# Kernel tuning notes

Measured on AMD Instinct MI355X. Metric: run time of the kernel, lower is better.

The kernel has to match this reference:

```python
import jax, jax.numpy as jnp
import numpy as np

EPS = 1e-6
NUM_HEADS = 8
NUM_TOKENS = 196

def setup_inputs() -> dict:
    key = jax.random.key(0)
    ks = jax.random.split(key, 4)
    B, N, C = 32, 3136, 384
    H, Dh, M = NUM_HEADS, C // NUM_HEADS, NUM_TOKENS
    return {
        "x": jax.random.normal(ks[0], (B, N, C), dtype=jnp.float32),
        "q_param": jax.random.normal(ks[1], (1, M, H, Dh), dtype=jnp.float32) * 0.02,
        "kv_w": jax.random.normal(ks[2], (2 * C, C), dtype=jnp.float32) * 0.02,
        "proj_w": jax.random.normal(ks[3], (C, C), dtype=jnp.float32) * 0.02,
        "proj_b": jnp.zeros((C,), dtype=jnp.float32),
        "ln_w": jnp.ones((C,), dtype=jnp.float32),
        "ln_b": jnp.zeros((C,), dtype=jnp.float32),
    }

def reference(x, q_param, kv_w, proj_w, proj_b, ln_w, ln_b):
    B, N, C = x.shape
    H = NUM_HEADS
    Dh = C // H
    # LayerNorm (eps=1e-6)
    mu = jnp.mean(x, axis=-1, keepdims=True)
    var = jnp.mean(jnp.square(x - mu), axis=-1, keepdims=True)
    x = (x - mu) * jax.lax.rsqrt(var + EPS) * ln_w + ln_b
    # exact GELU (nn.GELU default)
    x = jax.nn.gelu(x, approximate=False)
    # kv projection (no bias): [B,N,2C] -> k,v each [B,H,N,Dh]
    kv = (x @ kv_w.T).reshape(B, N, 2, H, Dh)
    kv = jnp.transpose(kv, (2, 0, 3, 1, 4))
    k, v = kv[0], kv[1]
    # learnable queries: (1,M,H,Dh) -> (1,H,M,Dh)
    q = jnp.transpose(q_param, (0, 2, 1, 3))
    # NOTE: source applies NO 1/sqrt(Dh) scaling
    attn = jnp.einsum("bhmd,bhnd->bhmn", jnp.broadcast_to(q, (B, H, NUM_TOKENS, Dh)), k)
    attn = jax.nn.softmax(attn, axis=-1)
    out = jnp.einsum("bhmn,bhnd->bhmd", attn, v)  # [B,H,M,Dh]
    out = jnp.transpose(out, (0, 2, 1, 3)).reshape(B, NUM_TOKENS, C)
    return out @ proj_w.T + proj_b
```

## Files before the change

### kernel.cpp

```cpp
#include <hip/hip_runtime.h>
#include <stdint.h>

typedef float f32x4 __attribute__((ext_vector_type(4)));
typedef short s16x8 __attribute__((ext_vector_type(8)));
typedef short s16x4 __attribute__((ext_vector_type(4)));
typedef unsigned short ushort_t;

#define B_  32
#define N_  3136
#define C_  384
#define H_  8
#define DH_ 48
#define M_  196
#define ROWS  (B_*N_)
#define PROWS (B_*M_)

static __device__ __forceinline__ ushort_t f2bf(float f) {
  union { float f; uint32_t u; } v; v.f = f;
  uint32_t r = (v.u + 0x7fffu + ((v.u >> 16) & 1u)) >> 16;
  return (ushort_t)r;
}
static __device__ __forceinline__ ushort_t f2bf_fast(float f) {
  union { float f; uint32_t u; } v; v.f = f;
  return (ushort_t)((v.u + 0x8000u) >> 16);
}
static __device__ __forceinline__ uint32_t pkbf(float lo, float hi) {
  uint32_t r;
  asm("v_cvt_pk_bf16_f32 %0, %1, %2" : "=v"(r) : "v"(lo), "v"(hi));
  return r;
}

static __device__ __forceinline__ f32x4 mfma_16x16x32(s16x8 a, s16x8 b, f32x4 c) {
  return __builtin_amdgcn_mfma_f32_16x16x32_bf16(a, b, c, 0, 0, 0);
}

static __device__ __forceinline__ f32x4 mfma_16x16x16(s16x4 a, s16x4 b, f32x4 c) {
#if __has_builtin(__builtin_amdgcn_mfma_f32_16x16x16_bf16)
  return __builtin_amdgcn_mfma_f32_16x16x16_bf16(a, b, c, 0, 0, 0);
#elif __has_builtin(__builtin_amdgcn_mfma_f32_16x16x16bf16_1k)
  return __builtin_amdgcn_mfma_f32_16x16x16bf16_1k(a, b, c, 0, 0, 0);
#else
  f32x4 d;
  asm("v_mfma_f32_16x16x16_bf16 %0, %1, %2, %3" : "=v"(d) : "v"(a), "v"(b), "v"(c));
  return d;
#endif
}

static __device__ __forceinline__ void gload_lds16(const void* g, void* l) {
  __builtin_amdgcn_global_load_lds(
      (const __attribute__((address_space(1))) void*)(uintptr_t)g,
      (__attribute__((address_space(3))) void*)(uint32_t)(uintptr_t)l,
      16, 0, 0);
}

__global__ __launch_bounds__(256) void k_ln_gelu(
    const float* __restrict__ x, const float* __restrict__ lnw,
    const float* __restrict__ lnb, ushort_t* __restrict__ x16) {
  int row = blockIdx.x * 4 + (threadIdx.x >> 6);
  int lane = threadIdx.x & 63;
  const float2* xr = (const float2*)(x + (size_t)row * C_);
  float2 v0 = xr[lane], v1 = xr[lane + 64], v2 = xr[lane + 128];
  float s  = v0.x + v0.y + v1.x + v1.y + v2.x + v2.y;
  float ss = v0.x*v0.x + v0.y*v0.y + v1.x*v1.x + v1.y*v1.y + v2.x*v2.x + v2.y*v2.y;
#pragma unroll
  for (int off = 1; off < 64; off <<= 1) {
    s  += __shfl_xor(s, off);
    ss += __shfl_xor(ss, off);
  }
  float mu = s * (1.0f / C_);
  float rs = rsqrtf(ss * (1.0f / C_) - mu * mu + 1e-6f);
  const float2* wr = (const float2*)lnw;
  const float2* br = (const float2*)lnb;
  uint32_t* outp = (uint32_t*)(x16 + (size_t)row * C_);
#pragma unroll
  for (int t = 0; t < 3; ++t) {
    int idx = lane + t * 64;
    float2 v = (t == 0) ? v0 : ((t == 1) ? v1 : v2);
    float2 w = wr[idx], bb = br[idx];
    float a0 = (v.x - mu) * rs * w.x + bb.x;
    float a1 = (v.y - mu) * rs * w.y + bb.y;
    a0 = 0.5f * a0 * (1.0f + erff(a0 * 0.70710678118654752440f));
    a1 = 0.5f * a1 * (1.0f + erff(a1 * 0.70710678118654752440f));
    outp[idx] = (uint32_t)f2bf_fast(a0) | ((uint32_t)f2bf_fast(a1) << 16);
  }
}

__global__ __launch_bounds__(256) void k_convert(
    const float* __restrict__ kvw, const float* __restrict__ pw,
    const float* __restrict__ qp, ushort_t* __restrict__ wkv16,
    ushort_t* __restrict__ wp16, ushort_t* __restrict__ q16) {
  int i = blockIdx.x * 256 + threadIdx.x;
  if (i < 2 * C_ * C_) wkv16[i] = f2bf(kvw[i]);
  if (i < C_ * C_)     wp16[i]  = f2bf(pw[i]);
  if (i < M_ * H_ * DH_) {
    int d = i % DH_; int t = i / DH_; int h = t % H_; int m = t / H_;
    q16[((size_t)h * M_ + m) * DH_ + d] = f2bf(qp[i]);
  }
}

template <typename OutT, bool BIAS, bool SWZ>
__global__ __launch_bounds__(256) void k_gemm_bt(
    const ushort_t* __restrict__ A, const ushort_t* __restrict__ Bw,
    OutT* __restrict__ Co, const float* __restrict__ bias,
    int M, int N, int K, int ntn) {
  __shared__ ushort_t lA[3][128 * 32];
  __shared__ ushort_t lB[3][128 * 32];
  int bid = blockIdx.x;
  if (SWZ) bid = (bid & 7) * (gridDim.x >> 3) + (bid >> 3);
  int tr = bid / ntn, tc = bid % ntn;
  int tid = threadIdx.x;
  int w = tid >> 6, l = tid & 63;
  int wr = w >> 1, wc = w & 1;
  int c = l & 15, g = l >> 4;
  f32x4 acc[4][4];
#pragma unroll
  for (int i = 0; i < 4; ++i)
#pragma unroll
    for (int j = 0; j < 4; ++j) acc[i][j] = (f32x4){0.f, 0.f, 0.f, 0.f};
  const size_t a0 = (size_t)tr * 128, b0 = (size_t)tc * 128;
  int srow = l >> 2;
  int scol = (((l & 3) ^ ((l >> 3) & 3))) * 8;
  const int rsw = (c >> 1) & 3;
  const int T = K >> 5;
#pragma unroll
  for (int r = 0; r < 2; ++r) {
    int lr = w * 16 + r * 64;
    gload_lds16(A  + (a0 + lr + srow) * (size_t)K + scol, &lA[0][lr * 32]);
    gload_lds16(Bw + (b0 + lr + srow) * (size_t)K + scol, &lB[0][lr * 32]);
  }
  if (T > 1) {
#pragma unroll
    for (int r = 0; r < 2; ++r) {
      int lr = w * 16 + r * 64;
      gload_lds16(A  + (a0 + lr + srow) * (size_t)K + 32 + scol, &lA[1][lr * 32]);
      gload_lds16(Bw + (b0 + lr + srow) * (size_t)K + 32 + scol, &lB[1][lr * 32]);
    }
  }
  int cur = 0, nxt2 = 2;
  for (int t = 0; t < T; ++t) {
    if (t + 2 < T) {
      int kt = (t + 2) << 5;
#pragma unroll
      for (int r = 0; r < 2; ++r) {
        int lr = w * 16 + r * 64;
        gload_lds16(A  + (a0 + lr + srow) * (size_t)K + kt + scol, &lA[nxt2][lr * 32]);
        gload_lds16(Bw + (b0 + lr + srow) * (size_t)K + kt + scol, &lB[nxt2][lr * 32]);
      }
      asm volatile("s_waitcnt vmcnt(8)" ::: "memory");
    } else if (t + 1 < T) {
      asm volatile("s_waitcnt vmcnt(4)" ::: "memory");
    } else {
      asm volatile("s_waitcnt vmcnt(0)" ::: "memory");
    }
    __builtin_amdgcn_sched_barrier(0);
    __builtin_amdgcn_s_barrier();
    s16x8 af[4], bf[4];
#pragma unroll
    for (int i = 0; i < 4; ++i) {
      int row = wr * 64 + i * 16 + c;
      af[i] = *(const s16x8*)&lA[cur][row * 32 + ((unsigned)(g ^ rsw)) * 8];
    }
#pragma unroll
    for (int j = 0; j < 4; ++j) {
      int row = wc * 64 + j * 16 + c;
      bf[j] = *(const s16x8*)&lB[cur][row * 32 + ((unsigned)(g ^ rsw)) * 8];
    }
#pragma unroll
    for (int i = 0; i < 4; ++i)
#pragma unroll
      for (int j = 0; j < 4; ++j)
        acc[i][j] = mfma_16x16x32(af[i], bf[j], acc[i][j]);
    __builtin_amdgcn_sched_barrier(0);
    __builtin_amdgcn_s_barrier();
    cur = (cur == 2) ? 0 : cur + 1;
    nxt2 = (nxt2 == 2) ? 0 : nxt2 + 1;
  }
#pragma unroll
  for (int i = 0; i < 4; ++i) {
#pragma unroll
    for (int j = 0; j < 4; ++j) {
      size_t col = b0 + wc * 64 + j * 16 + c;
      float bs = BIAS ? bias[col] : 0.0f;
#pragma unroll
      for (int q = 0; q < 4; ++q) {
        size_t row = a0 + wr * 64 + i * 16 + g * 4 + q;
        float v = acc[i][j][q] + bs;
        if constexpr (sizeof(OutT) == 2) Co[row * N + col] = f2bf(v);
        else                             Co[row * N + col] = v;
      }
    }
  }
}

__global__ __launch_bounds__(512) void k_attn(
    const ushort_t* __restrict__ kv, const ushort_t* __restrict__ q16,
    ushort_t* __restrict__ att16) {
  int bh = blockIdx.x;
  int b = bh >> 3, h = bh & 7;
  __shared__ ushort_t Kl[2][64 * 72];
  __shared__ ushort_t Vt[2][48 * 76];
  int tid = threadIdx.x;
  int w = tid >> 6, l = tid & 63;
  int c = l & 15, g = l >> 4;
  for (int i = tid; i < 2 * 64 * 72; i += 512) ((ushort_t*)Kl)[i] = 0;
  s16x8 qf[2][2];
#pragma unroll
  for (int i = 0; i < 2; ++i)
#pragma unroll
    for (int kk = 0; kk < 2; ++kk) {
      int m = w * 32 + i * 16 + c;
      int dh = kk * 32 + g * 8;
      s16x8 z = {0, 0, 0, 0, 0, 0, 0, 0};
      qf[i][kk] = (m < M_ && dh < DH_)
                      ? *(const s16x8*)(q16 + ((size_t)h * M_ + m) * DH_ + dh)
                      : z;
    }
  f32x4 o[3][2];
#pragma unroll
  for (int f = 0; f < 3; ++f)
#pragma unroll
    for (int i = 0; i < 2; ++i) o[f][i] = (f32x4){0.f, 0.f, 0.f, 0.f};
  float rm[2] = {-3e38f, -3e38f}, rl[2] = {0.f, 0.f};
  int srow = tid >> 3, spart = tid & 7;
  const size_t rowstride = (size_t)(2 * C_);
  const size_t gbase = (size_t)b * N_ * rowstride + h * DH_ + spart * 6;
  uint32_t kr0, kr1, kr2, vr0, vr1, vr2;
  {
    const ushort_t* p = kv + gbase + (size_t)srow * rowstride;
    kr0 = *(const uint32_t*)(p);
    kr1 = *(const uint32_t*)(p + 2);
    kr2 = *(const uint32_t*)(p + 4);
    vr0 = *(const uint32_t*)(p + C_);
    vr1 = *(const uint32_t*)(p + C_ + 2);
    vr2 = *(const uint32_t*)(p + C_ + 4);
  }
  __syncthreads();

  for (int t = 0; t < 49; ++t) {
    int p = t & 1;
    uint32_t* kd = (uint32_t*)&Kl[p][srow * 72 + spart * 6];
    kd[0] = kr0; kd[1] = kr1; kd[2] = kr2;
    int dbase = spart * 6;
    ushort_t* vt = &Vt[p][0];
    vt[(dbase + 0) * 76 + srow] = (ushort_t)vr0;
    vt[(dbase + 1) * 76 + srow] = (ushort_t)(vr0 >> 16);
    vt[(dbase + 2) * 76 + srow] = (ushort_t)vr1;
    vt[(dbase + 3) * 76 + srow] = (ushort_t)(vr1 >> 16);
    vt[(dbase + 4) * 76 + srow] = (ushort_t)vr2;
    vt[(dbase + 5) * 76 + srow] = (ushort_t)(vr2 >> 16);
    __syncthreads();
    {
      int tn = (t < 48) ? t + 1 : t;
      const ushort_t* pp = kv + gbase + ((size_t)tn * 64 + srow) * rowstride;
      kr0 = *(const uint32_t*)(pp);
      kr1 = *(const uint32_t*)(pp + 2);
      kr2 = *(const uint32_t*)(pp + 4);
      vr0 = *(const uint32_t*)(pp + C_);
      vr1 = *(const uint32_t*)(pp + C_ + 2);
      vr2 = *(const uint32_t*)(pp + C_ + 4);
    }
    f32x4 s[4][2];
    __builtin_amdgcn_s_setprio(1);
#pragma unroll
    for (int j = 0; j < 4; ++j) {
      s16x8 kf0 = *(const s16x8*)&Kl[p][(j * 16 + c) * 72 + g * 8];
      s16x8 kf1 = *(const s16x8*)&Kl[p][(j * 16 + c) * 72 + 32 + g * 8];
#pragma unroll
      for (int i = 0; i < 2; ++i) {
        f32x4 z = {0.f, 0.f, 0.f, 0.f};
        f32x4 t0 = mfma_16x16x32(kf0, qf[i][0], z);
        s[j][i] = mfma_16x16x32(kf1, qf[i][1], t0);
      }
    }
    __builtin_amdgcn_s_setprio(0);
    s16x4 pb[2][4];
#pragma unroll
    for (int i = 0; i < 2; ++i) {
      float tm = s[0][i][0];
#pragma unroll
      for (int j = 0; j < 4; ++j)
#pragma unroll
        for (int q = 0; q < 4; ++q) tm = fmaxf(tm, s[j][i][q]);
      tm = fmaxf(tm, __shfl_xor(tm, 16));
      tm = fmaxf(tm, __shfl_xor(tm, 32));
      if (__any(tm > rm[i] + 8.f)) {
        float nm = fmaxf(rm[i], tm);
        float corr = __expf(rm[i] - nm);
        rl[i] *= corr;
#pragma unroll
        for (int f = 0; f < 3; ++f) o[f][i] *= corr;
        rm[i] = nm;
      }
      float m_i = rm[i];
      float ts = 0.f;
#pragma unroll
      for (int j = 0; j < 4; ++j) {
        float p0 = __expf(s[j][i][0] - m_i);
        float p1 = __expf(s[j][i][1] - m_i);
        float p2 = __expf(s[j][i][2] - m_i);
        float p3 = __expf(s[j][i][3] - m_i);
        ts += (p0 + p1) + (p2 + p3);
        uint32_t* pp = (uint32_t*)&pb[i][j];
        pp[0] = pkbf(p0, p1);
        pp[1] = pkbf(p2, p3);
      }
      ts += __shfl_xor(ts, 16);
      ts += __shfl_xor(ts, 32);
      rl[i] += ts;
    }
    __builtin_amdgcn_s_setprio(1);
#pragma unroll
    for (int f = 0; f < 3; ++f)
#pragma unroll
      for (int j = 0; j < 4; ++j) {
        s16x4 vf = *(const s16x4*)&Vt[p][(f * 16 + c) * 76 + j * 16 + g * 4];
        o[f][0] = mfma_16x16x16(vf, pb[0][j], o[f][0]);
        o[f][1] = mfma_16x16x16(vf, pb[1][j], o[f][1]);
      }
    __builtin_amdgcn_s_setprio(0);
  }
#pragma unroll
  for (int i = 0; i < 2; ++i) {
    int m = w * 32 + i * 16 + c;
    if (m < M_) {
      float inv = 1.0f / rl[i];
#pragma unroll
      for (int f = 0; f < 3; ++f) {
        uint32_t w0 = (uint32_t)f2bf_fast(o[f][i][0] * inv) |
                      ((uint32_t)f2bf_fast(o[f][i][1] * inv) << 16);
        uint32_t w1 = (uint32_t)f2bf_fast(o[f][i][2] * inv) |
                      ((uint32_t)f2bf_fast(o[f][i][3] * inv) << 16);
        uint2 val; val.x = w0; val.y = w1;
        *(uint2*)&att16[((size_t)b * M_ + m) * C_ + h * DH_ + f * 16 + g * 4] = val;
      }
    }
  }
}

extern "C" void kernel_launch(void* const* d_in, const int* in_sizes, int n_in,
                              void* d_out, int out_size, void* d_ws, size_t ws_size,
                              hipStream_t stream) {
  (void)in_sizes; (void)n_in; (void)out_size; (void)ws_size;
  const float* x   = (const float*)d_in[0];
  const float* qp  = (const float*)d_in[1];
  const float* kvw = (const float*)d_in[2];
  const float* pw  = (const float*)d_in[3];
  const float* pbv = (const float*)d_in[4];
  const float* lnw = (const float*)d_in[5];
  const float* lnb = (const float*)d_in[6];
  float* out = (float*)d_out;

  ushort_t* x16   = (ushort_t*)d_ws;
  ushort_t* kv16  = x16 + (size_t)ROWS * C_;
  ushort_t* att16 = kv16 + (size_t)ROWS * 2 * C_;
  ushort_t* wkv16 = att16 + (size_t)PROWS * C_;
  ushort_t* wp16  = wkv16 + 2 * C_ * C_;
  ushort_t* q16   = wp16 + C_ * C_;

  hipLaunchKernelGGL(k_ln_gelu, dim3(ROWS / 4), dim3(256), 0, stream, x, lnw, lnb, x16);
  hipLaunchKernelGGL(k_convert, dim3((2 * C_ * C_ + 255) / 256), dim3(256), 0, stream,
                     kvw, pw, qp, wkv16, wp16, q16);
  hipLaunchKernelGGL((k_gemm_bt<ushort_t, false, true>),
                     dim3((ROWS / 128) * (2 * C_ / 128)), dim3(256), 0, stream,
                     x16, wkv16, kv16, (const float*)nullptr, ROWS, 2 * C_, C_, 2 * C_ / 128);
  hipLaunchKernelGGL(k_attn, dim3(B_ * H_), dim3(512), 0, stream, kv16, q16, att16);
  hipLaunchKernelGGL((k_gemm_bt<float, true, false>),
                     dim3((PROWS / 128) * (C_ / 128)), dim3(256), 0, stream,
                     att16, wp16, out, pbv, PROWS, C_, C_, C_ / 128);
}
```

Baseline: 248.7 us.

## Use 64-wide K tiles with double buffering in GEMM; skip idle attention wave

The GEMM kernel moves from a three-stage pipeline of 32-wide K tiles to a two-stage pipeline of 64-wide K tiles, with a new XOR swizzle over 8 column chunks. Each barrier pair now covers two MFMA k-steps, which halves the synchronisation per unit of work at the cost of a shallower prefetch. In the attention kernel, wave 7 (query rows 224 and up, past M=196) skips the QK, softmax and PV compute but still takes part in loads and barriers, removing wasted MFMA and exp work.

```diff
diff --git a/kernel.cpp b/kernel.cpp
--- a/kernel.cpp
+++ b/kernel.cpp
@@ -103,8 +103,8 @@
     const ushort_t* __restrict__ A, const ushort_t* __restrict__ Bw,
     OutT* __restrict__ Co, const float* __restrict__ bias,
     int M, int N, int K, int ntn) {
-  __shared__ ushort_t lA[3][128 * 32];
-  __shared__ ushort_t lB[3][128 * 32];
+  __shared__ ushort_t lA[2][128 * 64];
+  __shared__ ushort_t lB[2][128 * 64];
   int bid = blockIdx.x;
   if (SWZ) bid = (bid & 7) * (gridDim.x >> 3) + (bid >> 3);
   int tr = bid / ntn, tc = bid % ntn;
@@ -118,63 +118,55 @@
 #pragma unroll
     for (int j = 0; j < 4; ++j) acc[i][j] = (f32x4){0.f, 0.f, 0.f, 0.f};
   const size_t a0 = (size_t)tr * 128, b0 = (size_t)tc * 128;
-  int srow = l >> 2;
-  int scol = (((l & 3) ^ ((l >> 3) & 3))) * 8;
-  const int rsw = (c >> 1) & 3;
-  const int T = K >> 5;
-#pragma unroll
-  for (int r = 0; r < 2; ++r) {
-    int lr = w * 16 + r * 64;
-    gload_lds16(A  + (a0 + lr + srow) * (size_t)K + scol, &lA[0][lr * 32]);
-    gload_lds16(Bw + (b0 + lr + srow) * (size_t)K + scol, &lB[0][lr * 32]);
-  }
-  if (T > 1) {
-#pragma unroll
-    for (int r = 0; r < 2; ++r) {
-      int lr = w * 16 + r * 64;
-      gload_lds16(A  + (a0 + lr + srow) * (size_t)K + 32 + scol, &lA[1][lr * 32]);
-      gload_lds16(Bw + (b0 + lr + srow) * (size_t)K + 32 + scol, &lB[1][lr * 32]);
-    }
-  }
-  int cur = 0, nxt2 = 2;
+  int srow8 = l >> 3, scb = l & 7;
+  int ssrc = (scb ^ srow8) * 8;
+  const int c7 = c & 7;
+  const int T = K >> 6;
+#define STAGE_TILE(buf, kt)                                                        \
+  {                                                                                \
+    _Pragma("unroll")                                                              \
+    for (int r = 0; r < 4; ++r) {                                                  \
+      int row = w * 8 + r * 32 + srow8;                                            \
+      gload_lds16(A  + (a0 + row) * (size_t)K + (kt) + ssrc,                       \
+                  &lA[buf][w * 512 + r * 2048]);                                   \
+      gload_lds16(Bw + (b0 + row) * (size_t)K + (kt) + ssrc,                       \
+                  &lB[buf][w * 512 + r * 2048]);                                   \
+    }                                                                              \
+  }
+  STAGE_TILE(0, 0)
   for (int t = 0; t < T; ++t) {
-    if (t + 2 < T) {
-      int kt = (t + 2) << 5;
-#pragma unroll
-      for (int r = 0; r < 2; ++r) {
-        int lr = w * 16 + r * 64;
-        gload_lds16(A  + (a0 + lr + srow) * (size_t)K + kt + scol, &lA[nxt2][lr * 32]);
-        gload_lds16(Bw + (b0 + lr + srow) * (size_t)K + kt + scol, &lB[nxt2][lr * 32]);
-      }
+    int cur = t & 1;
+    if (t + 1 < T) {
+      STAGE_TILE(cur ^ 1, (t + 1) << 6)
       asm volatile("s_waitcnt vmcnt(8)" ::: "memory");
-    } else if (t + 1 < T) {
-      asm volatile("s_waitcnt vmcnt(4)" ::: "memory");
     } else {
       asm volatile("s_waitcnt vmcnt(0)" ::: "memory");
     }
     __builtin_amdgcn_sched_barrier(0);
     __builtin_amdgcn_s_barrier();
-    s16x8 af[4], bf[4];
-#pragma unroll
-    for (int i = 0; i < 4; ++i) {
-      int row = wr * 64 + i * 16 + c;
-      af[i] = *(const s16x8*)&lA[cur][row * 32 + ((unsigned)(g ^ rsw)) * 8];
-    }
-#pragma unroll
-    for (int j = 0; j < 4; ++j) {
-      int row = wc * 64 + j * 16 + c;
-      bf[j] = *(const s16x8*)&lB[cur][row * 32 + ((unsigned)(g ^ rsw)) * 8];
-    }
-#pragma unroll
-    for (int i = 0; i < 4; ++i)
-#pragma unroll
-      for (int j = 0; j < 4; ++j)
-        acc[i][j] = mfma_16x16x32(af[i], bf[j], acc[i][j]);
+#pragma unroll
+    for (int kk = 0; kk < 2; ++kk) {
+      s16x8 af[4], bf[4];
+#pragma unroll
+      for (int i = 0; i < 4; ++i) {
+        int row = wr * 64 + i * 16 + c;
+        af[i] = *(const s16x8*)&lA[cur][row * 64 + (((kk * 4 + g) ^ c7) * 8)];
+      }
+#pragma unroll
+      for (int j = 0; j < 4; ++j) {
+        int row = wc * 64 + j * 16 + c;
+        bf[j] = *(const s16x8*)&lB[cur][row * 64 + (((kk * 4 + g) ^ c7) * 8)];
+      }
+#pragma unroll
+      for (int i = 0; i < 4; ++i)
+#pragma unroll
+        for (int j = 0; j < 4; ++j)
+          acc[i][j] = mfma_16x16x32(af[i], bf[j], acc[i][j]);
+    }
     __builtin_amdgcn_sched_barrier(0);
     __builtin_amdgcn_s_barrier();
-    cur = (cur == 2) ? 0 : cur + 1;
-    nxt2 = (nxt2 == 2) ? 0 : nxt2 + 1;
-  }
+  }
+#undef STAGE_TILE
 #pragma unroll
   for (int i = 0; i < 4; ++i) {
 #pragma unroll
@@ -259,65 +251,67 @@
       vr1 = *(const uint32_t*)(pp + C_ + 2);
       vr2 = *(const uint32_t*)(pp + C_ + 4);
     }
-    f32x4 s[4][2];
-    __builtin_amdgcn_s_setprio(1);
-#pragma unroll
-    for (int j = 0; j < 4; ++j) {
-      s16x8 kf0 = *(const s16x8*)&Kl[p][(j * 16 + c) * 72 + g * 8];
-      s16x8 kf1 = *(const s16x8*)&Kl[p][(j * 16 + c) * 72 + 32 + g * 8];
+    if (w < 7) {
+      f32x4 s[4][2];
+      __builtin_amdgcn_s_setprio(1);
+#pragma unroll
+      for (int j = 0; j < 4; ++j) {
+        s16x8 kf0 = *(const s16x8*)&Kl[p][(j * 16 + c) * 72 + g * 8];
+        s16x8 kf1 = *(const s16x8*)&Kl[p][(j * 16 + c) * 72 + 32 + g * 8];
+#pragma unroll
+        for (int i = 0; i < 2; ++i) {
+          f32x4 z = {0.f, 0.f, 0.f, 0.f};
+          f32x4 t0 = mfma_16x16x32(kf0, qf[i][0], z);
+          s[j][i] = mfma_16x16x32(kf1, qf[i][1], t0);
+        }
+      }
+      __builtin_amdgcn_s_setprio(0);
+      s16x4 pb[2][4];
 #pragma unroll
       for (int i = 0; i < 2; ++i) {
-        f32x4 z = {0.f, 0.f, 0.f, 0.f};
-        f32x4 t0 = mfma_16x16x32(kf0, qf[i][0], z);
-        s[j][i] = mfma_16x16x32(kf1, qf[i][1], t0);
-      }
-    }
-    __builtin_amdgcn_s_setprio(0);
-    s16x4 pb[2][4];
-#pragma unroll
-    for (int i = 0; i < 2; ++i) {
-      float tm = s[0][i][0];
-#pragma unroll
-      for (int j = 0; j < 4; ++j)
-#pragma unroll
-        for (int q = 0; q < 4; ++q) tm = fmaxf(tm, s[j][i][q]);
-      tm = fmaxf(tm, __shfl_xor(tm, 16));
-      tm = fmaxf(tm, __shfl_xor(tm, 32));
-      if (__any(tm > rm[i] + 8.f)) {
-        float nm = fmaxf(rm[i], tm);
-        float corr = __expf(rm[i] - nm);
-        rl[i] *= corr;
-#pragma unroll
-        for (int f = 0; f < 3; ++f) o[f][i] *= corr;
-        rm[i] = nm;
-      }
-      float m_i = rm[i];
-      float ts = 0.f;
-#pragma unroll
-      for (int j = 0; j < 4; ++j) {
-        float p0 = __expf(s[j][i][0] - m_i);
-        float p1 = __expf(s[j][i][1] - m_i);
-        float p2 = __expf(s[j][i][2] - m_i);
-        float p3 = __expf(s[j][i][3] - m_i);
-        ts += (p0 + p1) + (p2 + p3);
-        uint32_t* pp = (uint32_t*)&pb[i][j];
-        pp[0] = pkbf(p0, p1);
-        pp[1] = pkbf(p2, p3);
-      }
-      ts += __shfl_xor(ts, 16);
-      ts += __shfl_xor(ts, 32);
-      rl[i] += ts;
-    }
-    __builtin_amdgcn_s_setprio(1);
-#pragma unroll
-    for (int f = 0; f < 3; ++f)
-#pragma unroll
-      for (int j = 0; j < 4; ++j) {
-        s16x4 vf = *(const s16x4*)&Vt[p][(f * 16 + c) * 76 + j * 16 + g * 4];
-        o[f][0] = mfma_16x16x16(vf, pb[0][j], o[f][0]);
-        o[f][1] = mfma_16x16x16(vf, pb[1][j], o[f][1]);
-      }
-    __builtin_amdgcn_s_setprio(0);
+        float tm = s[0][i][0];
+#pragma unroll
+        for (int j = 0; j < 4; ++j)
+#pragma unroll
+          for (int q = 0; q < 4; ++q) tm = fmaxf(tm, s[j][i][q]);
+        tm = fmaxf(tm, __shfl_xor(tm, 16));
+        tm = fmaxf(tm, __shfl_xor(tm, 32));
+        if (__any(tm > rm[i] + 8.f)) {
+          float nm = fmaxf(rm[i], tm);
+          float corr = __expf(rm[i] - nm);
+          rl[i] *= corr;
+#pragma unroll
+          for (int f = 0; f < 3; ++f) o[f][i] *= corr;
+          rm[i] = nm;
+        }
+        float m_i = rm[i];
+        float ts = 0.f;
+#pragma unroll
+        for (int j = 0; j < 4; ++j) {
+          float p0 = __expf(s[j][i][0] - m_i);
+          float p1 = __expf(s[j][i][1] - m_i);
+          float p2 = __expf(s[j][i][2] - m_i);
+          float p3 = __expf(s[j][i][3] - m_i);
+          ts += (p0 + p1) + (p2 + p3);
+          uint32_t* pp = (uint32_t*)&pb[i][j];
+          pp[0] = pkbf(p0, p1);
+          pp[1] = pkbf(p2, p3);
+        }
+        ts += __shfl_xor(ts, 16);
+        ts += __shfl_xor(ts, 32);
+        rl[i] += ts;
+      }
+      __builtin_amdgcn_s_setprio(1);
+#pragma unroll
+      for (int f = 0; f < 3; ++f)
+#pragma unroll
+        for (int j = 0; j < 4; ++j) {
+          s16x4 vf = *(const s16x4*)&Vt[p][(f * 16 + c) * 76 + j * 16 + g * 4];
+          o[f][0] = mfma_16x16x16(vf, pb[0][j], o[f][0]);
+          o[f][1] = mfma_16x16x16(vf, pb[1][j], o[f][1]);
+        }
+      __builtin_amdgcn_s_setprio(0);
+    }
   }
 #pragma unroll
   for (int i = 0; i < 2; ++i) {
```

Result: no change. 248.4 us (-0.1%).
